# Kernel tuning notes

Measured on AMD Instinct MI355X. Metric: run time of the kernel, lower is better.

Reference implementation:

```python
import jax, jax.numpy as jnp
import numpy as np

DMODEL = 512
NUM_HEADS = 8
DK = DMODEL // NUM_HEADS  # 64
CAUSAL = True


def setup_inputs() -> dict:
    key = jax.random.key(0)
    ks = jax.random.split(key, 11)
    B, S = 4, 2048
    s_in = 1.0 / np.sqrt(DMODEL)
    s_out = 1.0 / np.sqrt(NUM_HEADS * DK)
    return {
        "Q": jax.random.normal(ks[0], (B, S, DMODEL), jnp.float32),
        "K": jax.random.normal(ks[1], (B, S, DMODEL), jnp.float32),
        "V": jax.random.normal(ks[2], (B, S, DMODEL), jnp.float32),
        # torch nn.Linear weights stored as [in, out] (already transposed)
        "WQ_w": jax.random.uniform(ks[3], (DMODEL, DK), jnp.float32, -s_in, s_in),
        "WQ_b": jax.random.uniform(ks[4], (DK,), jnp.float32, -s_in, s_in),
        "WK_w": jax.random.uniform(ks[5], (DMODEL, DK), jnp.float32, -s_in, s_in),
        "WK_b": jax.random.uniform(ks[6], (DK,), jnp.float32, -s_in, s_in),
        "WV_w": jax.random.uniform(ks[7], (DMODEL, DK), jnp.float32, -s_in, s_in),
        "WV_b": jax.random.uniform(ks[8], (DK,), jnp.float32, -s_in, s_in),
        "Wo_w": jax.random.uniform(ks[9], (NUM_HEADS * DK, DMODEL), jnp.float32, -s_out, s_out),
        "Wo_b": jax.random.uniform(ks[10], (DMODEL,), jnp.float32, -s_out, s_out),
    }


def reference(Q, K, V, WQ_w, WQ_b, WK_w, WK_b, WV_w, WV_b, Wo_w, Wo_b):
    # Single shared projection to dk=64 (NOT per-head in the original module)
    q = Q @ WQ_w + WQ_b  # [B,S,dk]
    k = K @ WK_w + WK_b  # [B,S,dk]
    v = V @ WV_w + WV_b  # [B,S,dk]
    scores = jnp.einsum("bsd,btd->bst", q, k) / np.sqrt(DK).astype(np.float32)
    if CAUSAL:
        S = scores.shape[-1]
        causal = jnp.tril(jnp.ones((S, S), dtype=bool))  # True = keep
        scores = jnp.where(causal, scores, -jnp.inf)
    attn = jax.nn.softmax(scores, axis=-1)
    head_out = jnp.einsum("bst,btd->bsd", attn, v)  # [B,S,dk]
    # Every head is identical -> concat == tile num_heads copies
    concat = jnp.tile(head_out, (1, 1, NUM_HEADS))  # [B,S,num_heads*dk]
    return concat @ Wo_w + Wo_b  # [B,S,dmodel]
```

## Files before the change

kernel.cpp:

```cpp
#include <hip/hip_runtime.h>

#define DMODEL 512
#define DK 64
#define NH 8
#define SEQ 2048
#define BATCH 4
#define NEGBIG -1.0e30f
#define SPLITW 8
#define DKP 66
#define XSP 520
#define SHIFT2 8.656170245f
#define QSCALE 0.1803368801f

typedef _Float16 half_t;
typedef _Float16 half4 __attribute__((ext_vector_type(4)));
typedef _Float16 half8 __attribute__((ext_vector_type(8)));
typedef float floatx4 __attribute__((ext_vector_type(4)));

#ifdef __has_builtin
#  if __has_builtin(__builtin_amdgcn_exp2f)
#    define EXP2F(x) __builtin_amdgcn_exp2f(x)
#  endif
#  if __has_builtin(__builtin_amdgcn_cvt_pkrtz)
#    define HAVE_PKRTZ 1
#  endif
#  if __has_builtin(__builtin_amdgcn_mfma_f32_16x16x16f16)
#    define HAVE_MFMA16 1
#  endif
#endif
#ifndef EXP2F
#  define EXP2F(x) exp2f(x)
#endif
#ifndef HAVE_PKRTZ
#  define HAVE_PKRTZ 0
#endif
#ifndef HAVE_MFMA16
#  define HAVE_MFMA16 0
#endif

__device__ __forceinline__ half4 pk4(const float* p) {
#if HAVE_PKRTZ
    half4 r;
    auto lo = __builtin_amdgcn_cvt_pkrtz(p[0], p[1]);
    auto hi = __builtin_amdgcn_cvt_pkrtz(p[2], p[3]);
    __builtin_memcpy(&r, &lo, 4);
    __builtin_memcpy(reinterpret_cast<char*>(&r) + 4, &hi, 4);
    return r;
#else
    return (half4){(half_t)p[0], (half_t)p[1], (half_t)p[2], (half_t)p[3]};
#endif
}

__global__ __launch_bounds__(128) void proj_kernel(
    const float* __restrict__ Q, const float* __restrict__ K, const float* __restrict__ V,
    const float* __restrict__ WQ, const float* __restrict__ WK, const float* __restrict__ WV,
    const float* __restrict__ Wo,
    const float* __restrict__ bQ, const float* __restrict__ bK, const float* __restrict__ bV,
    half_t* __restrict__ qh, half_t* __restrict__ kh, half_t* __restrict__ vt,
    half_t* __restrict__ wo_tr)
{
    const int tens = blockIdx.y;
    const int tid = threadIdx.x;

    if (tens == 3) {
        const int idx = blockIdx.x * 128 + tid;
        const int n2 = idx & 511;
        const int k2 = idx >> 9;
        float s = 0.f;
#pragma unroll
        for (int h = 0; h < NH; h++)
            s += Wo[((size_t)(h * DK + k2)) * DMODEL + n2];
        wo_tr[(size_t)n2 * DK + k2] = (half_t)s;
        return;
    }

    const float* __restrict__ X  = (tens == 0) ? Q : (tens == 1) ? K : V;
    const float* __restrict__ Wf = (tens == 0) ? WQ : (tens == 1) ? WK : WV;
    const float* __restrict__ bias = (tens == 0) ? bQ : (tens == 1) ? bK : bV;

    const int r0 = blockIdx.x * 32;
    const int w = tid >> 6;
    const int lane = tid & 63;
    const int c = lane & 15;
    const int quad = lane >> 4;

    __shared__ half_t xs[32][XSP];
    __shared__ floatx4 red[2][4][64];

    {
        const floatx4* __restrict__ Xv = (const floatx4*)(X + (size_t)r0 * DMODEL);
#pragma unroll
        for (int batch = 0; batch < 4; batch++) {
            floatx4 v[8];
#pragma unroll
            for (int j = 0; j < 8; j++)
                v[j] = __builtin_nontemporal_load(&Xv[(batch * 8 + j) * 128 + tid]);
#pragma unroll
            for (int j = 0; j < 8; j++) {
                const int fi = (batch * 8 + j) * 128 + tid;
                half_t* d = &xs[fi >> 7][(fi & 127) * 4];
                d[0] = (half_t)v[j][0]; d[1] = (half_t)v[j][1];
                d[2] = (half_t)v[j][2]; d[3] = (half_t)v[j][3];
            }
        }
    }
    __syncthreads();

    floatx4 acc[2][4] = {{{0.f,0.f,0.f,0.f},{0.f,0.f,0.f,0.f},{0.f,0.f,0.f,0.f},{0.f,0.f,0.f,0.f}},
                         {{0.f,0.f,0.f,0.f},{0.f,0.f,0.f,0.f},{0.f,0.f,0.f,0.f},{0.f,0.f,0.f,0.f}}};

#pragma unroll 8
    for (int ks = w; ks < 16; ks += 2) {
        const half8 a0 = *(const half8*)(&xs[c][ks * 32 + quad * 8]);
        const half8 a1 = *(const half8*)(&xs[16 + c][ks * 32 + quad * 8]);
        const float* wbase = Wf + (size_t)(ks * 32 + quad * 8) * DK + c;
#pragma unroll
        for (int nt = 0; nt < 4; nt++) {
            half8 bfr;
#pragma unroll
            for (int j = 0; j < 8; j++)
                bfr[j] = (half_t)wbase[(size_t)j * DK + nt * 16];
            acc[0][nt] = __builtin_amdgcn_mfma_f32_16x16x32_f16(a0, bfr, acc[0][nt], 0, 0, 0);
            acc[1][nt] = __builtin_amdgcn_mfma_f32_16x16x32_f16(a1, bfr, acc[1][nt], 0, 0, 0);
        }
    }

    if (w == 1) {
#pragma unroll
        for (int rt = 0; rt < 2; rt++)
#pragma unroll
            for (int nt = 0; nt < 4; nt++) red[rt][nt][lane] = acc[rt][nt];
    }
    __syncthreads();
    if (w == 1) return;

#pragma unroll
    for (int rt = 0; rt < 2; rt++) {
#pragma unroll
        for (int nt = 0; nt < 4; nt++) {
            const floatx4 r4 = red[rt][nt][lane];
            const float bv = bias[nt * 16 + c];
#pragma unroll
            for (int r = 0; r < 4; r++) {
                const float val = acc[rt][nt][r] + r4[r] + bv;
                const int row = r0 + rt * 16 + quad * 4 + r;
                if (tens == 0) {
                    qh[(size_t)row * DK + nt * 16 + c] = (half_t)(val * QSCALE);
                } else if (tens == 1) {
                    kh[(size_t)row * DK + nt * 16 + c] = (half_t)val;
                } else {
                    const int b  = row >> 11;
                    const int s  = row & (SEQ - 1);
                    const int kb = s >> 4;
                    const int kk = s & 15;
                    vt[(size_t)(b * 128 + kb) * 1024
                       + (size_t)c * 64 + (nt >> 1) * 32 + (kk >> 2) * 8 + (nt & 1) * 4 + (kk & 3)]
                        = (half_t)val;
                }
            }
        }
    }
}

__global__ __launch_bounds__(512, 4) void attn_kernel(
    const half_t* __restrict__ qh, const half_t* __restrict__ kh,
    const half_t* __restrict__ vt, const half_t* __restrict__ wo_tr,
    const float* __restrict__ bo, float* __restrict__ out)
{
    const int bx = blockIdx.x;
    int b, qt;
    if (bx < 256) { qt = bx >> 1;            b = bx & 1; }
    else          { int k2 = bx - 256; qt = 127 - (k2 >> 1); b = 2 + (k2 & 1); }
    const int tid = threadIdx.x;
    const int w = tid >> 6;
    const int lane = tid & 63;
    const int c = lane & 15;
    const int quad = lane >> 4;

    __shared__ float sow[SPLITW][16][DKP];
    __shared__ float sl_s[SPLITW][16];
    __shared__ half_t of16[16][72];

    const half_t* qrow = qh + (size_t)(b * SEQ + qt * 16 + c) * DK + quad * 8;
    half8 qb0 = *(const half8*)(qrow);
    half8 qb1 = *(const half8*)(qrow + 32);

    float lp = 0.f;
    floatx4 o[4] = {{0.f,0.f,0.f,0.f},{0.f,0.f,0.f,0.f},{0.f,0.f,0.f,0.f},{0.f,0.f,0.f,0.f}};
    const floatx4 cinit = {-SHIFT2, -SHIFT2, -SHIFT2, -SHIFT2};

    const half_t* kbb = kh + (size_t)b * SEQ * DK;
    const half_t* vtb = vt + (size_t)b * 128 * 1024;

    int pb = w;
    half8 ka0, ka1, kb0, kb1;
    if (2 * pb <= qt) {
        const half_t* kr0 = kbb + (size_t)(2 * pb * 16 + c) * DK + quad * 8;
        ka0 = *(const half8*)(kr0);
        ka1 = *(const half8*)(kr0 + 32);
        const half_t* kr1 = kr0 + 16 * DK;
        kb0 = *(const half8*)(kr1);
        kb1 = *(const half8*)(kr1 + 32);
    }

    while (2 * pb <= qt) {
        const int t0 = 2 * pb, t1 = 2 * pb + 1;
        const half_t* vp0 = vtb + (size_t)t0 * 1024 + c * 64 + quad * 8;
        const half_t* vp1 = vtb + (size_t)t1 * 1024 + c * 64 + quad * 8;
        half8 va01 = *(const half8*)(vp0);
        half8 va23 = *(const half8*)(vp0 + 32);
        half8 vc01 = *(const half8*)(vp1);
        half8 vc23 = *(const half8*)(vp1 + 32);

        const int npb = pb + SPLITW;
        half8 nka0 = ka0, nka1 = ka1, nkb0 = kb0, nkb1 = kb1;
        if (2 * npb <= qt) {
            const half_t* nkr0 = kbb + (size_t)(2 * npb * 16 + c) * DK + quad * 8;
            nka0 = *(const half8*)(nkr0);
            nka1 = *(const half8*)(nkr0 + 32);
            const half_t* nkr1 = nkr0 + 16 * DK;
            nkb0 = *(const half8*)(nkr1);
            nkb1 = *(const half8*)(nkr1 + 32);
        }

        floatx4 sc0 = cinit;
        sc0 = __builtin_amdgcn_mfma_f32_16x16x32_f16(ka0, qb0, sc0, 0, 0, 0);
        sc0 = __builtin_amdgcn_mfma_f32_16x16x32_f16(ka1, qb1, sc0, 0, 0, 0);
        floatx4 sc1 = cinit;
        sc1 = __builtin_amdgcn_mfma_f32_16x16x32_f16(kb0, qb0, sc1, 0, 0, 0);
        sc1 = __builtin_amdgcn_mfma_f32_16x16x32_f16(kb1, qb1, sc1, 0, 0, 0);

        if (t0 == qt) {
#pragma unroll
            for (int r = 0; r < 4; r++) {
                if (quad * 4 + r > c) sc0[r] = NEGBIG;
                sc1[r] = NEGBIG;
            }
        } else if (t1 == qt) {
#pragma unroll
            for (int r = 0; r < 4; r++)
                if (quad * 4 + r > c) sc1[r] = NEGBIG;
        }

        float p0[4], p1[4];
#pragma unroll
        for (int r = 0; r < 4; r++) { p0[r] = EXP2F(sc0[r]); p1[r] = EXP2F(sc1[r]); }
        lp += (p0[0] + p0[1]) + (p0[2] + p0[3]) + ((p1[0] + p1[1]) + (p1[2] + p1[3]));

#if HAVE_MFMA16
        half4 pa = pk4(p0), pc = pk4(p1);
        half4 va0 = __builtin_shufflevector(va01, va01, 0, 1, 2, 3);
        half4 va1 = __builtin_shufflevector(va01, va01, 4, 5, 6, 7);
        half4 va2 = __builtin_shufflevector(va23, va23, 0, 1, 2, 3);
        half4 va3 = __builtin_shufflevector(va23, va23, 4, 5, 6, 7);
        half4 vc0 = __builtin_shufflevector(vc01, vc01, 0, 1, 2, 3);
        half4 vc1 = __builtin_shufflevector(vc01, vc01, 4, 5, 6, 7);
        half4 vc2 = __builtin_shufflevector(vc23, vc23, 0, 1, 2, 3);
        half4 vc3 = __builtin_shufflevector(vc23, vc23, 4, 5, 6, 7);
        o[0] = __builtin_amdgcn_mfma_f32_16x16x16f16(pa, va0, o[0], 0, 0, 0);
        o[1] = __builtin_amdgcn_mfma_f32_16x16x16f16(pa, va1, o[1], 0, 0, 0);
        o[2] = __builtin_amdgcn_mfma_f32_16x16x16f16(pa, va2, o[2], 0, 0, 0);
        o[3] = __builtin_amdgcn_mfma_f32_16x16x16f16(pa, va3, o[3], 0, 0, 0);
        o[0] = __builtin_amdgcn_mfma_f32_16x16x16f16(pc, vc0, o[0], 0, 0, 0);
        o[1] = __builtin_amdgcn_mfma_f32_16x16x16f16(pc, vc1, o[1], 0, 0, 0);
        o[2] = __builtin_amdgcn_mfma_f32_16x16x16f16(pc, vc2, o[2], 0, 0, 0);
        o[3] = __builtin_amdgcn_mfma_f32_16x16x16f16(pc, vc3, o[3], 0, 0, 0);
#else
        half8 pa8, pc8;
#pragma unroll
        for (int jj = 0; jj < 8; jj++) {
            const int src = (((quad * 2 + (jj >> 2)) & 3) * 16 + c);
            const float pj0 = __shfl(p0[jj & 3], src);
            const float pj1 = __shfl(p1[jj & 3], src);
            pa8[jj] = (quad < 2) ? (half_t)pj0 : (half_t)0.f;
            pc8[jj] = (quad < 2) ? (half_t)pj1 : (half_t)0.f;
        }
#pragma unroll
        for (int nt = 0; nt < 4; nt++) {
            const half_t* vb0 = vtb + (size_t)t0 * 1024 + c * 64 + (nt >> 1) * 32 + (quad & 1) * 16 + (nt & 1) * 4;
            half4 l0 = *(const half4*)(vb0);
            half4 h0 = *(const half4*)(vb0 + 8);
            half8 v80 = {l0[0], l0[1], l0[2], l0[3], h0[0], h0[1], h0[2], h0[3]};
            o[nt] = __builtin_amdgcn_mfma_f32_16x16x32_f16(pa8, v80, o[nt], 0, 0, 0);
            const half_t* vb1 = vtb + (size_t)t1 * 1024 + c * 64 + (nt >> 1) * 32 + (quad & 1) * 16 + (nt & 1) * 4;
            half4 l1 = *(const half4*)(vb1);
            half4 h1 = *(const half4*)(vb1 + 8);
            half8 v81 = {l1[0], l1[1], l1[2], l1[3], h1[0], h1[1], h1[2], h1[3]};
            o[nt] = __builtin_amdgcn_mfma_f32_16x16x32_f16(pc8, v81, o[nt], 0, 0, 0);
        }
#endif
        ka0 = nka0; ka1 = nka1; kb0 = nkb0; kb1 = nkb1; pb = npb;
    }

    lp += __shfl_xor(lp, 16);
    lp += __shfl_xor(lp, 32);

#pragma unroll
    for (int nt = 0; nt < 4; nt++)
#pragma unroll
        for (int r = 0; r < 4; r++)
            sow[w][quad * 4 + r][nt * 16 + c] = o[nt][r];
    if (quad == 0) sl_s[w][c] = lp;
    __syncthreads();

    {
        const int q = w * 2 + (lane >> 5);
        const int d0 = (lane & 31) * 2;
        float lstar = 0.f, acc0 = 0.f, acc1 = 0.f;
#pragma unroll
        for (int ww = 0; ww < SPLITW; ww++) {
            lstar += sl_s[ww][q];
            const float* sp = &sow[ww][q][d0];
            acc0 += sp[0];
            acc1 += sp[1];
        }
        const float linv = 1.f / lstar;
        of16[q][d0]     = (half_t)(acc0 * linv);
        of16[q][d0 + 1] = (half_t)(acc1 * linv);
    }
    __syncthreads();

    half8 a1 = *(const half8*)(&of16[c][quad * 8]);
    half8 a2 = *(const half8*)(&of16[c][32 + quad * 8]);
    const size_t orow = (size_t)(b * SEQ + qt * 16);
#pragma unroll
    for (int i = 0; i < 4; i++) {
        const int n = (w * 4 + i) * 16 + c;
        half8 b1 = *(const half8*)(wo_tr + (size_t)n * DK + quad * 8);
        half8 b2 = *(const half8*)(wo_tr + (size_t)n * DK + 32 + quad * 8);
        floatx4 oc = {0.f, 0.f, 0.f, 0.f};
        oc = __builtin_amdgcn_mfma_f32_16x16x32_f16(a1, b1, oc, 0, 0, 0);
        oc = __builtin_amdgcn_mfma_f32_16x16x32_f16(a2, b2, oc, 0, 0, 0);
        const float bv = bo[n];
#pragma unroll
        for (int r = 0; r < 4; r++)
            __builtin_nontemporal_store(oc[r] + bv, &out[(orow + quad * 4 + r) * DMODEL + n]);
    }
}

extern "C" void kernel_launch(void* const* d_in, const int* in_sizes, int n_in,
                              void* d_out, int out_size, void* d_ws, size_t ws_size,
                              hipStream_t stream) {
    const float* Q  = (const float*)d_in[0];
    const float* K  = (const float*)d_in[1];
    const float* V  = (const float*)d_in[2];
    const float* WQ = (const float*)d_in[3];
    const float* bQ = (const float*)d_in[4];
    const float* WK = (const float*)d_in[5];
    const float* bK = (const float*)d_in[6];
    const float* WV = (const float*)d_in[7];
    const float* bV = (const float*)d_in[8];
    const float* Wo = (const float*)d_in[9];
    const float* bo = (const float*)d_in[10];
    float* out = (float*)d_out;

    char* ws = (char*)d_ws;
    half_t* qh    = (half_t*)ws;
    half_t* kh    = (half_t*)(ws + (1u << 20));
    half_t* vt    = (half_t*)(ws + (2u << 20));
    half_t* wo_tr = (half_t*)(ws + (3u << 20));

    proj_kernel<<<dim3(256, 4), 128, 0, stream>>>(
        Q, K, V, WQ, WK, WV, Wo, bQ, bK, bV, qh, kh, vt, wo_tr);
    attn_kernel<<<512, 512, 0, stream>>>(qh, kh, vt, wo_tr, bo, out);
}
```

Before: 136.4 us.

## Pair complementary causal query tiles per block with a 16-wave work queue

```diff
diff --git a/kernel.cpp b/kernel.cpp
--- a/kernel.cpp
+++ b/kernel.cpp
@@ -6,7 +6,7 @@
 #define SEQ 2048
 #define BATCH 4
 #define NEGBIG -1.0e30f
-#define SPLITW 8
+#define NWAVES 16
 #define DKP 66
 #define XSP 520
 #define SHIFT2 8.656170245f
@@ -162,39 +162,131 @@
     }
 }
 
-__global__ __launch_bounds__(512, 4) void attn_kernel(
+__device__ __forceinline__ void attn_item(
+    const int pb, const int qt,
+    const half8 qb0, const half8 qb1,
+    const half8 ka0, const half8 ka1, const half8 kb0, const half8 kb1,
+    const half_t* __restrict__ vtb,
+    floatx4 (&o)[4], float& lp,
+    const int c, const int quad)
+{
+    const int t0 = 2 * pb, t1 = 2 * pb + 1;
+    const half_t* vp0 = vtb + (size_t)t0 * 1024 + c * 64 + quad * 8;
+    const half_t* vp1 = vtb + (size_t)t1 * 1024 + c * 64 + quad * 8;
+    half8 va01 = *(const half8*)(vp0);
+    half8 va23 = *(const half8*)(vp0 + 32);
+    half8 vc01 = *(const half8*)(vp1);
+    half8 vc23 = *(const half8*)(vp1 + 32);
+
+    const floatx4 cinit = {-SHIFT2, -SHIFT2, -SHIFT2, -SHIFT2};
+    floatx4 sc0 = cinit;
+    sc0 = __builtin_amdgcn_mfma_f32_16x16x32_f16(ka0, qb0, sc0, 0, 0, 0);
+    sc0 = __builtin_amdgcn_mfma_f32_16x16x32_f16(ka1, qb1, sc0, 0, 0, 0);
+    floatx4 sc1 = cinit;
+    sc1 = __builtin_amdgcn_mfma_f32_16x16x32_f16(kb0, qb0, sc1, 0, 0, 0);
+    sc1 = __builtin_amdgcn_mfma_f32_16x16x32_f16(kb1, qb1, sc1, 0, 0, 0);
+
+    if (t0 == qt) {
+#pragma unroll
+        for (int r = 0; r < 4; r++) {
+            if (quad * 4 + r > c) sc0[r] = NEGBIG;
+            sc1[r] = NEGBIG;
+        }
+    } else if (t1 == qt) {
+#pragma unroll
+        for (int r = 0; r < 4; r++)
+            if (quad * 4 + r > c) sc1[r] = NEGBIG;
+    }
+
+    float p0[4], p1[4];
+#pragma unroll
+    for (int r = 0; r < 4; r++) { p0[r] = EXP2F(sc0[r]); p1[r] = EXP2F(sc1[r]); }
+    lp += (p0[0] + p0[1]) + (p0[2] + p0[3]) + ((p1[0] + p1[1]) + (p1[2] + p1[3]));
+
+#if HAVE_MFMA16
+    half4 pa = pk4(p0), pc = pk4(p1);
+    half4 va0 = __builtin_shufflevector(va01, va01, 0, 1, 2, 3);
+    half4 va1 = __builtin_shufflevector(va01, va01, 4, 5, 6, 7);
+    half4 va2 = __builtin_shufflevector(va23, va23, 0, 1, 2, 3);
+    half4 va3 = __builtin_shufflevector(va23, va23, 4, 5, 6, 7);
+    half4 vc0 = __builtin_shufflevector(vc01, vc01, 0, 1, 2, 3);
+    half4 vc1 = __builtin_shufflevector(vc01, vc01, 4, 5, 6, 7);
+    half4 vc2 = __builtin_shufflevector(vc23, vc23, 0, 1, 2, 3);
+    half4 vc3 = __builtin_shufflevector(vc23, vc23, 4, 5, 6, 7);
+    o[0] = __builtin_amdgcn_mfma_f32_16x16x16f16(pa, va0, o[0], 0, 0, 0);
+    o[1] = __builtin_amdgcn_mfma_f32_16x16x16f16(pa, va1, o[1], 0, 0, 0);
+    o[2] = __builtin_amdgcn_mfma_f32_16x16x16f16(pa, va2, o[2], 0, 0, 0);
+    o[3] = __builtin_amdgcn_mfma_f32_16x16x16f16(pa, va3, o[3], 0, 0, 0);
+    o[0] = __builtin_amdgcn_mfma_f32_16x16x16f16(pc, vc0, o[0], 0, 0, 0);
+    o[1] = __builtin_amdgcn_mfma_f32_16x16x16f16(pc, vc1, o[1], 0, 0, 0);
+    o[2] = __builtin_amdgcn_mfma_f32_16x16x16f16(pc, vc2, o[2], 0, 0, 0);
+    o[3] = __builtin_amdgcn_mfma_f32_16x16x16f16(pc, vc3, o[3], 0, 0, 0);
+#else
+    half8 pa8, pc8;
+#pragma unroll
+    for (int jj = 0; jj < 8; jj++) {
+        const int src = (((quad * 2 + (jj >> 2)) & 3) * 16 + c);
+        const float pj0 = __shfl(p0[jj & 3], src);
+        const float pj1 = __shfl(p1[jj & 3], src);
+        pa8[jj] = (quad < 2) ? (half_t)pj0 : (half_t)0.f;
+        pc8[jj] = (quad < 2) ? (half_t)pj1 : (half_t)0.f;
+    }
+#pragma unroll
+    for (int nt = 0; nt < 4; nt++) {
+        const half_t* vb0 = vtb + (size_t)t0 * 1024 + c * 64 + (nt >> 1) * 32 + (quad & 1) * 16 + (nt & 1) * 4;
+        half4 l0 = *(const half4*)(vb0);
+        half4 h0 = *(const half4*)(vb0 + 8);
+        half8 v80 = {l0[0], l0[1], l0[2], l0[3], h0[0], h0[1], h0[2], h0[3]};
+        o[nt] = __builtin_amdgcn_mfma_f32_16x16x32_f16(pa8, v80, o[nt], 0, 0, 0);
+        const half_t* vb1 = vtb + (size_t)t1 * 1024 + c * 64 + (nt >> 1) * 32 + (quad & 1) * 16 + (nt & 1) * 4;
+        half4 l1 = *(const half4*)(vb1);
+        half4 h1 = *(const half4*)(vb1 + 8);
+        half8 v81 = {l1[0], l1[1], l1[2], l1[3], h1[0], h1[1], h1[2], h1[3]};
+        o[nt] = __builtin_amdgcn_mfma_f32_16x16x32_f16(pc8, v81, o[nt], 0, 0, 0);
+    }
+#endif
+}
+
+__global__ __launch_bounds__(1024, 4) void attn_kernel(
     const half_t* __restrict__ qh, const half_t* __restrict__ kh,
     const half_t* __restrict__ vt, const half_t* __restrict__ wo_tr,
     const float* __restrict__ bo, float* __restrict__ out)
 {
-    const int bx = blockIdx.x;
-    int b, qt;
-    if (bx < 256) { qt = bx >> 1;            b = bx & 1; }
-    else          { int k2 = bx - 256; qt = 127 - (k2 >> 1); b = 2 + (k2 & 1); }
+    const int bx  = blockIdx.x;
+    const int b   = bx & 3;
+    const int qtA = bx >> 2;
+    const int qtB = 127 - qtA;
+    const int Pa  = (qtA >> 1) + 1;
+    const int Pb  = (qtB >> 1) + 1;
+    const int nitems = Pa + Pb;
     const int tid = threadIdx.x;
     const int w = tid >> 6;
     const int lane = tid & 63;
     const int c = lane & 15;
     const int quad = lane >> 4;
 
-    __shared__ float sow[SPLITW][16][DKP];
-    __shared__ float sl_s[SPLITW][16];
-    __shared__ half_t of16[16][72];
-
-    const half_t* qrow = qh + (size_t)(b * SEQ + qt * 16 + c) * DK + quad * 8;
-    half8 qb0 = *(const half8*)(qrow);
-    half8 qb1 = *(const half8*)(qrow + 32);
-
-    float lp = 0.f;
-    floatx4 o[4] = {{0.f,0.f,0.f,0.f},{0.f,0.f,0.f,0.f},{0.f,0.f,0.f,0.f},{0.f,0.f,0.f,0.f}};
-    const floatx4 cinit = {-SHIFT2, -SHIFT2, -SHIFT2, -SHIFT2};
+    __shared__ float sow[2][NWAVES][16][DKP];
+    __shared__ float sl_s[2][NWAVES][16];
+    __shared__ half_t of16[2][16][72];
+
+    const half_t* qrowA = qh + (size_t)(b * SEQ + qtA * 16 + c) * DK + quad * 8;
+    const half8 qbA0 = *(const half8*)(qrowA);
+    const half8 qbA1 = *(const half8*)(qrowA + 32);
+    const half_t* qrowB = qh + (size_t)(b * SEQ + qtB * 16 + c) * DK + quad * 8;
+    const half8 qbB0 = *(const half8*)(qrowB);
+    const half8 qbB1 = *(const half8*)(qrowB + 32);
+
+    float lpA = 0.f, lpB = 0.f;
+    floatx4 oA[4] = {{0.f,0.f,0.f,0.f},{0.f,0.f,0.f,0.f},{0.f,0.f,0.f,0.f},{0.f,0.f,0.f,0.f}};
+    floatx4 oB[4] = {{0.f,0.f,0.f,0.f},{0.f,0.f,0.f,0.f},{0.f,0.f,0.f,0.f},{0.f,0.f,0.f,0.f}};
 
     const half_t* kbb = kh + (size_t)b * SEQ * DK;
     const half_t* vtb = vt + (size_t)b * 128 * 1024;
 
-    int pb = w;
+    int item = w;
     half8 ka0, ka1, kb0, kb1;
-    if (2 * pb <= qt) {
+    if (item < nitems) {
+        const int pb = (item < Pa) ? item : item - Pa;
         const half_t* kr0 = kbb + (size_t)(2 * pb * 16 + c) * DK + quad * 8;
         ka0 = *(const half8*)(kr0);
         ka1 = *(const half8*)(kr0 + 32);
@@ -203,18 +295,12 @@
         kb1 = *(const half8*)(kr1 + 32);
     }
 
-    while (2 * pb <= qt) {
-        const int t0 = 2 * pb, t1 = 2 * pb + 1;
-        const half_t* vp0 = vtb + (size_t)t0 * 1024 + c * 64 + quad * 8;
-        const half_t* vp1 = vtb + (size_t)t1 * 1024 + c * 64 + quad * 8;
-        half8 va01 = *(const half8*)(vp0);
-        half8 va23 = *(const half8*)(vp0 + 32);
-        half8 vc01 = *(const half8*)(vp1);
-        half8 vc23 = *(const half8*)(vp1 + 32);
-
-        const int npb = pb + SPLITW;
+    while (item < nitems) {
+        const int pb = (item < Pa) ? item : item - Pa;
+        const int nitem = item + NWAVES;
         half8 nka0 = ka0, nka1 = ka1, nkb0 = kb0, nkb1 = kb1;
-        if (2 * npb <= qt) {
+        if (nitem < nitems) {
+            const int npb = (nitem < Pa) ? nitem : nitem - Pa;
             const half_t* nkr0 = kbb + (size_t)(2 * npb * 16 + c) * DK + quad * 8;
             nka0 = *(const half8*)(nkr0);
             nka1 = *(const half8*)(nkr0 + 32);
@@ -222,119 +308,66 @@
             nkb0 = *(const half8*)(nkr1);
             nkb1 = *(const half8*)(nkr1 + 32);
         }
-
-        floatx4 sc0 = cinit;
-        sc0 = __builtin_amdgcn_mfma_f32_16x16x32_f16(ka0, qb0, sc0, 0, 0, 0);
-        sc0 = __builtin_amdgcn_mfma_f32_16x16x32_f16(ka1, qb1, sc0, 0, 0, 0);
-        floatx4 sc1 = cinit;
-        sc1 = __builtin_amdgcn_mfma_f32_16x16x32_f16(kb0, qb0, sc1, 0, 0, 0);
-        sc1 = __builtin_amdgcn_mfma_f32_16x16x32_f16(kb1, qb1, sc1, 0, 0, 0);
-
-        if (t0 == qt) {
-#pragma unroll
-            for (int r = 0; r < 4; r++) {
-                if (quad * 4 + r > c) sc0[r] = NEGBIG;
-                sc1[r] = NEGBIG;
-            }
-        } else if (t1 == qt) {
-#pragma unroll
-            for (int r = 0; r < 4; r++)
-                if (quad * 4 + r > c) sc1[r] = NEGBIG;
-        }
-
-        float p0[4], p1[4];
-#pragma unroll
-        for (int r = 0; r < 4; r++) { p0[r] = EXP2F(sc0[r]); p1[r] = EXP2F(sc1[r]); }
-        lp += (p0[0] + p0[1]) + (p0[2] + p0[3]) + ((p1[0] + p1[1]) + (p1[2] + p1[3]));
-
-#if HAVE_MFMA16
-        half4 pa = pk4(p0), pc = pk4(p1);
-        half4 va0 = __builtin_shufflevector(va01, va01, 0, 1, 2, 3);
-        half4 va1 = __builtin_shufflevector(va01, va01, 4, 5, 6, 7);
-        half4 va2 = __builtin_shufflevector(va23, va23, 0, 1, 2, 3);
-        half4 va3 = __builtin_shufflevector(va23, va23, 4, 5, 6, 7);
-        half4 vc0 = __builtin_shufflevector(vc01, vc01, 0, 1, 2, 3);
-        half4 vc1 = __builtin_shufflevector(vc01, vc01, 4, 5, 6, 7);
-        half4 vc2 = __builtin_shufflevector(vc23, vc23, 0, 1, 2, 3);
-        half4 vc3 = __builtin_shufflevector(vc23, vc23, 4, 5, 6, 7);
-        o[0] = __builtin_amdgcn_mfma_f32_16x16x16f16(pa, va0, o[0], 0, 0, 0);
-        o[1] = __builtin_amdgcn_mfma_f32_16x16x16f16(pa, va1, o[1], 0, 0, 0);
-        o[2] = __builtin_amdgcn_mfma_f32_16x16x16f16(pa, va2, o[2], 0, 0, 0);
-        o[3] = __builtin_amdgcn_mfma_f32_16x16x16f16(pa, va3, o[3], 0, 0, 0);
-        o[0] = __builtin_amdgcn_mfma_f32_16x16x16f16(pc, vc0, o[0], 0, 0, 0);
-        o[1] = __builtin_amdgcn_mfma_f32_16x16x16f16(pc, vc1, o[1], 0, 0, 0);
-        o[2] = __builtin_amdgcn_mfma_f32_16x16x16f16(pc, vc2, o[2], 0, 0, 0);
-        o[3] = __builtin_amdgcn_mfma_f32_16x16x16f16(pc, vc3, o[3], 0, 0, 0);
-#else
-        half8 pa8, pc8;
-#pragma unroll
-        for (int jj = 0; jj < 8; jj++) {
-            const int src = (((quad * 2 + (jj >> 2)) & 3) * 16 + c);
-            const float pj0 = __shfl(p0[jj & 3], src);
-            const float pj1 = __shfl(p1[jj & 3], src);
-            pa8[jj] = (quad < 2) ? (half_t)pj0 : (half_t)0.f;
-            pc8[jj] = (quad < 2) ? (half_t)pj1 : (half_t)0.f;
-        }
-#pragma unroll
-        for (int nt = 0; nt < 4; nt++) {
-            const half_t* vb0 = vtb + (size_t)t0 * 1024 + c * 64 + (nt >> 1) * 32 + (quad & 1) * 16 + (nt & 1) * 4;
-            half4 l0 = *(const half4*)(vb0);
-            half4 h0 = *(const half4*)(vb0 + 8);
-            half8 v80 = {l0[0], l0[1], l0[2], l0[3], h0[0], h0[1], h0[2], h0[3]};
-            o[nt] = __builtin_amdgcn_mfma_f32_16x16x32_f16(pa8, v80, o[nt], 0, 0, 0);
-            const half_t* vb1 = vtb + (size_t)t1 * 1024 + c * 64 + (nt >> 1) * 32 + (quad & 1) * 16 + (nt & 1) * 4;
-            half4 l1 = *(const half4*)(vb1);
-            half4 h1 = *(const half4*)(vb1 + 8);
-            half8 v81 = {l1[0], l1[1], l1[2], l1[3], h1[0], h1[1], h1[2], h1[3]};
-            o[nt] = __builtin_amdgcn_mfma_f32_16x16x32_f16(pc8, v81, o[nt], 0, 0, 0);
-        }
-#endif
-        ka0 = nka0; ka1 = nka1; kb0 = nkb0; kb1 = nkb1; pb = npb;
-    }
-
-    lp += __shfl_xor(lp, 16);
-    lp += __shfl_xor(lp, 32);
+        if (item < Pa)
+            attn_item(pb, qtA, qbA0, qbA1, ka0, ka1, kb0, kb1, vtb, oA, lpA, c, quad);
+        else
+            attn_item(pb, qtB, qbB0, qbB1, ka0, ka1, kb0, kb1, vtb, oB, lpB, c, quad);
+        ka0 = nka0; ka1 = nka1; kb0 = nkb0; kb1 = nkb1; item = nitem;
+    }
+
+    lpA += __shfl_xor(lpA, 16);
+    lpA += __shfl_xor(lpA, 32);
+    lpB += __shfl_xor(lpB, 16);
+    lpB += __shfl_xor(lpB, 32);
 
 #pragma unroll
     for (int nt = 0; nt < 4; nt++)
 #pragma unroll
-        for (int r = 0; r < 4; r++)
-            sow[w][quad * 4 + r][nt * 16 + c] = o[nt][r];
-    if (quad == 0) sl_s[w][c] = lp;
+        for (int r = 0; r < 4; r++) {
+            sow[0][w][quad * 4 + r][nt * 16 + c] = oA[nt][r];
+            sow[1][w][quad * 4 + r][nt * 16 + c] = oB[nt][r];
+        }
+    if (quad == 0) { sl_s[0][w][c] = lpA; sl_s[1][w][c] = lpB; }
     __syncthreads();
 
     {
-        const int q = w * 2 + (lane >> 5);
-        const int d0 = (lane & 31) * 2;
+        const int tile = tid >> 9;
+        const int q = (tid >> 5) & 15;
+        const int d0 = (tid & 31) * 2;
         float lstar = 0.f, acc0 = 0.f, acc1 = 0.f;
 #pragma unroll
-        for (int ww = 0; ww < SPLITW; ww++) {
-            lstar += sl_s[ww][q];
-            const float* sp = &sow[ww][q][d0];
+        for (int ww = 0; ww < NWAVES; ww++) {
+            lstar += sl_s[tile][ww][q];
+            const float* sp = &sow[tile][ww][q][d0];
             acc0 += sp[0];
             acc1 += sp[1];
         }
         const float linv = 1.f / lstar;
-        of16[q][d0]     = (half_t)(acc0 * linv);
-        of16[q][d0 + 1] = (half_t)(acc1 * linv);
+        of16[tile][q][d0]     = (half_t)(acc0 * linv);
+        of16[tile][q][d0 + 1] = (half_t)(acc1 * linv);
     }
     __syncthreads();
 
-    half8 a1 = *(const half8*)(&of16[c][quad * 8]);
-    half8 a2 = *(const half8*)(&of16[c][32 + quad * 8]);
-    const size_t orow = (size_t)(b * SEQ + qt * 16);
-#pragma unroll
-    for (int i = 0; i < 4; i++) {
-        const int n = (w * 4 + i) * 16 + c;
-        half8 b1 = *(const half8*)(wo_tr + (size_t)n * DK + quad * 8);
-        half8 b2 = *(const half8*)(wo_tr + (size_t)n * DK + 32 + quad * 8);
-        floatx4 oc = {0.f, 0.f, 0.f, 0.f};
-        oc = __builtin_amdgcn_mfma_f32_16x16x32_f16(a1, b1, oc, 0, 0, 0);
-        oc = __builtin_amdgcn_mfma_f32_16x16x32_f16(a2, b2, oc, 0, 0, 0);
-        const float bv = bo[n];
-#pragma unroll
-        for (int r = 0; r < 4; r++)
-            __builtin_nontemporal_store(oc[r] + bv, &out[(orow + quad * 4 + r) * DMODEL + n]);
+    {
+        const int tile = w >> 3;
+        const int wloc = w & 7;
+        const int qtT = tile ? qtB : qtA;
+        half8 a1 = *(const half8*)(&of16[tile][c][quad * 8]);
+        half8 a2 = *(const half8*)(&of16[tile][c][32 + quad * 8]);
+        const size_t orow = (size_t)(b * SEQ + qtT * 16);
+#pragma unroll
+        for (int i = 0; i < 4; i++) {
+            const int n = (wloc * 4 + i) * 16 + c;
+            half8 b1 = *(const half8*)(wo_tr + (size_t)n * DK + quad * 8);
+            half8 b2 = *(const half8*)(wo_tr + (size_t)n * DK + 32 + quad * 8);
+            floatx4 oc = {0.f, 0.f, 0.f, 0.f};
+            oc = __builtin_amdgcn_mfma_f32_16x16x32_f16(a1, b1, oc, 0, 0, 0);
+            oc = __builtin_amdgcn_mfma_f32_16x16x32_f16(a2, b2, oc, 0, 0, 0);
+            const float bv = bo[n];
+#pragma unroll
+            for (int r = 0; r < 4; r++)
+                __builtin_nontemporal_store(oc[r] + bv, &out[(orow + quad * 4 + r) * DMODEL + n]);
+        }
     }
 }
 
@@ -362,5 +395,5 @@
 
     proj_kernel<<<dim3(256, 4), 128, 0, stream>>>(
         Q, K, V, WQ, WK, WV, Wo, bQ, bK, bV, qh, kh, vt, wo_tr);
-    attn_kernel<<<512, 512, 0, stream>>>(qh, kh, vt, wo_tr, bo, out);
-}
+    attn_kernel<<<256, 1024, 0, stream>>>(qh, kh, vt, wo_tr, bo, out);
+}
```

After: 136.6 us. About the same (+0.1%).
